# Optimization experiments

Hardware: AMD Instinct MI355X
Metric: run time of the kernel (lower is better)

## Reference

```python
import jax, jax.numpy as jnp
import numpy as np
from jax import lax

B, T, C = 4, 4096, 2048
H, Dh = 16, 128          # num_heads, head_dim
K = 4                    # depthwise conv kernel
LN_EPS = 1e-5
NORM_EPS = 1e-12         # F.normalize eps


def setup_inputs() -> dict:
    key = jax.random.key(0)
    ks = jax.random.split(key, 9)
    s = 0.02
    x = jax.random.normal(ks[0], (B, T, C), jnp.float32)
    Wq = jax.random.normal(ks[1], (C, C), jnp.float32) * s  # torch Linear weight [out,in]
    Wk = jax.random.normal(ks[2], (C, C), jnp.float32) * s
    Wv = jax.random.normal(ks[3], (C, C), jnp.float32) * s
    Wo = jax.random.normal(ks[4], (C, C), jnp.float32) * s
    conv_w = jax.random.normal(ks[5], (C, 1, K), jnp.float32) * 0.2  # depthwise [O, I/groups, K]
    conv_b = jax.random.normal(ks[6], (C,), jnp.float32) * s
    gate_w = jax.random.normal(ks[7], (C, C), jnp.float32) * s
    gate_b = jnp.zeros((C,), jnp.float32)                   # gate_bias_init = 0.0
    ln_w = jnp.ones((C,), jnp.float32)
    ln_b = jnp.zeros((C,), jnp.float32)
    g = jnp.linspace(0.9, 0.999, H, dtype=jnp.float32).at[0].set(1.0)
    gamma = g.reshape(1, 1, H, 1)                           # non-trainable buffer
    return {"x": x, "Wq": Wq, "Wk": Wk, "Wv": Wv, "Wo": Wo,
            "conv_w": conv_w, "conv_b": conv_b, "gate_w": gate_w, "gate_b": gate_b,
            "ln_w": ln_w, "ln_b": ln_b, "gamma": gamma}


def _l2norm(t):
    n = jnp.linalg.norm(t, axis=-1, keepdims=True)
    return t / jnp.maximum(n, NORM_EPS)


def reference(x, Wq, Wk, Wv, Wo, conv_w, conv_b, gate_w, gate_b, ln_w, ln_b, gamma):
    b, t, c = x.shape
    # causal depthwise conv (torch pads K-1 both sides then slices [:T] == left-pad K-1)
    xc = lax.conv_general_dilated(
        jnp.swapaxes(x, 1, 2), conv_w, window_strides=(1,), padding=[(K - 1, 0)],
        feature_group_count=c, dimension_numbers=("NCH", "OIH", "NCH"))
    x_conv = jax.nn.silu(jnp.swapaxes(xc + conv_b[None, :, None], 1, 2))  # [B,T,C]

    q = jnp.einsum("btc,dc->btd", x, Wq).reshape(b, t, H, Dh)
    k = jnp.einsum("btc,dc->btd", x, Wk).reshape(b, t, H, Dh)
    v = jnp.einsum("btc,dc->btd", x, Wv).reshape(b, t, H, Dh)
    gate = jax.nn.sigmoid(jnp.einsum("btc,dc->btd", x_conv, gate_w) + gate_b)
    gate = gate.reshape(b, t, H, Dh)

    q = _l2norm(q)
    k = _l2norm(k)

    # elementwise decayed scan: S_t = gamma * S_{t-1} + k_t * v_t ; mem_t = gate_t * S_t
    kv = jnp.swapaxes(k * v, 0, 1)          # [T,B,H,Dh]
    g = gamma.reshape(1, H, 1)

    def step(S, kv_t):
        S = g * S + kv_t
        return S, S

    _, S_seq = lax.scan(step, jnp.zeros((b, H, Dh), x.dtype), kv)
    mem = gate * jnp.swapaxes(S_seq, 0, 1)  # [B,T,H,Dh]

    out = (mem * q).reshape(b, t, c)
    y = jnp.einsum("btc,dc->btd", out, Wo)
    mu = jnp.mean(y, axis=-1, keepdims=True)
    var = jnp.mean(jnp.square(y - mu), axis=-1, keepdims=True)
    return (y - mu) * lax.rsqrt(var + LN_EPS) * ln_w + ln_b
```

## Files before the change

kernel.cpp:

```cpp
#include <hip/hip_runtime.h>
#include <cstdint>

#define Bb 4
#define Tt 4096
#define Cc 2048
#define Hh 16
#define Dh 128
#define BT (Bb * Tt)
#define NCHUNK 32
#define TCHUNK 128
#define NCHAN (Bb * Cc)
#define NQKV 6144

typedef __bf16 bf16x8 __attribute__((ext_vector_type(8)));
typedef float f32x4 __attribute__((ext_vector_type(4)));
typedef unsigned short u16x8 __attribute__((ext_vector_type(8)));

__device__ __forceinline__ float bf2f(unsigned short u) {
  return __uint_as_float(((unsigned)u) << 16);
}
__device__ __forceinline__ unsigned short f2bf(float f) {
  unsigned u = __float_as_uint(f);
  u = u + 0x7fffu + ((u >> 16) & 1u);
  return (unsigned short)(u >> 16);
}

__device__ __forceinline__ void async_copy16(void* lds, const void* gmem) {
  auto* lp = (__attribute__((address_space(3))) unsigned int*)(unsigned)(uintptr_t)(lds);
  auto* gp = (const __attribute__((address_space(1))) unsigned int*)(uintptr_t)(gmem);
  __builtin_amdgcn_global_load_lds(gp, lp, 16, 0, 0);
}

__global__ __launch_bounds__(256) void cvt5_kernel(const float* __restrict__ Wq,
                                                   const float* __restrict__ Wk,
                                                   const float* __restrict__ Wv,
                                                   const float* __restrict__ Wo,
                                                   const float* __restrict__ Wg,
                                                   unsigned short* __restrict__ dst) {
  size_t idx4 = ((size_t)blockIdx.x * 256 + threadIdx.x) * 4;
  int region = (int)(idx4 >> 22);
  size_t off = idx4 & ((1u << 22) - 1);
  const float* src;
  switch (region) {
    case 0: src = Wq; break;
    case 1: src = Wk; break;
    case 2: src = Wv; break;
    case 3: src = Wo; break;
    default: src = Wg; break;
  }
  float4 v = *(const float4*)(src + off);
  unsigned r0 = (unsigned)f2bf(v.x) | ((unsigned)f2bf(v.y) << 16);
  unsigned r1 = (unsigned)f2bf(v.z) | ((unsigned)f2bf(v.w) << 16);
  *(uint2*)(dst + idx4) = make_uint2(r0, r1);
}

__global__ __launch_bounds__(256) void conv_kernel(const float* __restrict__ x,
                                                   const float* __restrict__ cw,
                                                   const float* __restrict__ cb,
                                                   unsigned short* __restrict__ xb,
                                                   unsigned short* __restrict__ xcb) {
  int idx = blockIdx.x * 256 + threadIdx.x;
  int cg = idx & 511;
  int rg = idx >> 9;
  int c = cg * 4;
  size_t bt0 = (size_t)rg * 8;
  int t0 = (int)(bt0 & (Tt - 1));
  const float* xp = x + bt0 * Cc + c;

  float4 w4[4];
#pragma unroll
  for (int u = 0; u < 4; u++) w4[u] = *(const float4*)(cw + (size_t)(c + u) * 4);
  float4 bias = *(const float4*)(cb + c);
  const float* bs = (const float*)&bias;

  float xr[11][4];
  if (t0 != 0) {
#pragma unroll
    for (int j = 0; j < 3; j++) {
      float4 p = *(const float4*)(xp - (size_t)(3 - j) * Cc);
      xr[j][0] = p.x; xr[j][1] = p.y; xr[j][2] = p.z; xr[j][3] = p.w;
    }
  } else {
#pragma unroll
    for (int j = 0; j < 3; j++)
#pragma unroll
      for (int u = 0; u < 4; u++) xr[j][u] = 0.f;
  }
#pragma unroll
  for (int i = 0; i < 8; i++) {
    float4 p = *(const float4*)(xp + (size_t)i * Cc);
    xr[3 + i][0] = p.x; xr[3 + i][1] = p.y; xr[3 + i][2] = p.z; xr[3 + i][3] = p.w;
    unsigned a0 = (unsigned)f2bf(p.x) | ((unsigned)f2bf(p.y) << 16);
    unsigned a1 = (unsigned)f2bf(p.z) | ((unsigned)f2bf(p.w) << 16);
    *(uint2*)(xb + (bt0 + i) * Cc + c) = make_uint2(a0, a1);
  }
#pragma unroll
  for (int i = 0; i < 8; i++) {
    unsigned short o[4];
#pragma unroll
    for (int u = 0; u < 4; u++) {
      const float* wf = (const float*)&w4[u];
      float a = bs[u];
#pragma unroll
      for (int j = 0; j < 4; j++) a += wf[3 - j] * xr[3 + i - j][u];
      float sig = 1.f / (1.f + expf(-a));
      o[u] = f2bf(a * sig);
    }
    unsigned q0 = (unsigned)o[0] | ((unsigned)o[1] << 16);
    unsigned q1 = (unsigned)o[2] | ((unsigned)o[3] << 16);
    *(uint2*)(xcb + (bt0 + i) * Cc + c) = make_uint2(q0, q1);
  }
}

template <int EPI>
__global__ __launch_bounds__(512, 2) void gemm256(const unsigned short* __restrict__ A,
                                                  const unsigned short* __restrict__ B,
                                                  void* __restrict__ C,
                                                  const float* __restrict__ bias,
                                                  int M, int N, int K) {
  __shared__ unsigned short As[4][256 * 32];
  __shared__ unsigned short Bs[4][256 * 32];
  __shared__ float rowsq[256][4];

  const int tid = threadIdx.x;
  const int w = tid >> 6;
  const int lane = tid & 63;

  const int nwg = gridDim.x * gridDim.y;
  const int flat = blockIdx.y * gridDim.x + blockIdx.x;
  const int cpx = nwg >> 3;
  const int swz = (flat & 7) * cpx + (flat >> 3);
  const int bx = swz % gridDim.x;
  const int by = swz / gridDim.x;
  const int m0 = bx * 256;
  const int n0 = by * 256;

  const int wr = w >> 2;
  const int wc = w & 3;

  const int srow = lane >> 2;
  const int scol = (((lane & 3) ^ ((lane >> 3) & 3)) << 3);
  const int r16 = w * 2;
  const unsigned short* Ag0 = A + (size_t)(m0 + r16 * 16 + srow) * K + scol;
  const unsigned short* Ag1 = Ag0 + (size_t)16 * K;
  const unsigned short* Bg0 = B + (size_t)(n0 + r16 * 16 + srow) * K + scol;
  const unsigned short* Bg1 = Bg0 + (size_t)16 * K;

  const int frow = lane & 15;
  const int cbs = ((((lane >> 4) << 4) ^ (((frow >> 1) & 3) << 4)) >> 1);

  f32x4 acc[8][4] = {};
  const int NT = K >> 5;

  {
    unsigned short* dA0 = &As[0][r16 * 512];
    unsigned short* dB0 = &Bs[0][r16 * 512];
    async_copy16(dA0, Ag0); async_copy16(dA0 + 512, Ag1);
    async_copy16(dB0, Bg0); async_copy16(dB0 + 512, Bg1);
    unsigned short* dA1 = &As[1][r16 * 512];
    unsigned short* dB1 = &Bs[1][r16 * 512];
    async_copy16(dA1, Ag0 + 32); async_copy16(dA1 + 512, Ag1 + 32);
    async_copy16(dB1, Bg0 + 32); async_copy16(dB1 + 512, Bg1 + 32);
  }
  asm volatile("s_waitcnt vmcnt(4)" ::: "memory");
  __builtin_amdgcn_s_barrier();

  for (int t = 0; t < NT; ++t) {
    const int slot = t & 3;
    const unsigned short* as = &As[slot][0] + wr * 4096 + cbs;
    const unsigned short* bsb = &Bs[slot][0] + wc * 2048 + cbs;
    const bool pf = (t + 2 < NT);
    const int kpf = (t + 2) << 5;

    bf16x8 af[4], bf[4];
#pragma unroll
    for (int m = 0; m < 4; m++)
      af[m] = __builtin_bit_cast(bf16x8, *(const u16x8*)(as + (m * 16 + frow) * 32));
#pragma unroll
    for (int n = 0; n < 4; n++)
      bf[n] = __builtin_bit_cast(bf16x8, *(const u16x8*)(bsb + (n * 16 + frow) * 32));
    if (pf) {
      unsigned short* d = &As[(t + 2) & 3][r16 * 512];
      async_copy16(d, Ag0 + kpf);
      async_copy16(d + 512, Ag1 + kpf);
    }
    __builtin_amdgcn_s_barrier();
    asm volatile("s_waitcnt lgkmcnt(0)" ::: "memory");
    __builtin_amdgcn_sched_barrier(0);
    __builtin_amdgcn_s_setprio(1);
#pragma unroll
    for (int m = 0; m < 4; m++)
#pragma unroll
      for (int n = 0; n < 4; n++)
        acc[m][n] = __builtin_amdgcn_mfma_f32_16x16x32_bf16(af[m], bf[n], acc[m][n], 0, 0, 0);
    __builtin_amdgcn_s_setprio(0);
    __builtin_amdgcn_s_barrier();

#pragma unroll
    for (int m = 0; m < 4; m++)
      af[m] = __builtin_bit_cast(bf16x8, *(const u16x8*)(as + ((m + 4) * 16 + frow) * 32));
    if (pf) {
      unsigned short* d = &Bs[(t + 2) & 3][r16 * 512];
      async_copy16(d, Bg0 + kpf);
      async_copy16(d + 512, Bg1 + kpf);
    }
    __builtin_amdgcn_s_barrier();
    asm volatile("s_waitcnt lgkmcnt(0)" ::: "memory");
    __builtin_amdgcn_sched_barrier(0);
    __builtin_amdgcn_s_setprio(1);
#pragma unroll
    for (int m = 0; m < 4; m++)
#pragma unroll
      for (int n = 0; n < 4; n++)
        acc[m + 4][n] = __builtin_amdgcn_mfma_f32_16x16x32_bf16(af[m], bf[n], acc[m + 4][n], 0, 0, 0);
    __builtin_amdgcn_s_setprio(0);
    if (pf) asm volatile("s_waitcnt vmcnt(4)" ::: "memory");
    else    asm volatile("s_waitcnt vmcnt(0)" ::: "memory");
    __builtin_amdgcn_s_barrier();
  }

  const int crow0 = (lane >> 4) * 4;
  const int ccol = lane & 15;

  float inv[8][4];
  const bool donorm = (EPI == 3) && (n0 < 2 * Cc);
  if (donorm) {
#pragma unroll
    for (int m = 0; m < 8; m++) {
#pragma unroll
      for (int r = 0; r < 4; r++) {
        float sq = 0.f;
#pragma unroll
        for (int n = 0; n < 4; n++) { float v = acc[m][n][r]; sq += v * v; }
        sq += __shfl_xor(sq, 1);
        sq += __shfl_xor(sq, 2);
        sq += __shfl_xor(sq, 4);
        sq += __shfl_xor(sq, 8);
        if (ccol == 0) rowsq[wr * 128 + m * 16 + crow0 + r][wc] = sq;
      }
    }
    __syncthreads();
#pragma unroll
    for (int m = 0; m < 8; m++)
#pragma unroll
      for (int r = 0; r < 4; r++) {
        int rloc = wr * 128 + m * 16 + crow0 + r;
        int g2 = (wc >> 1) * 2;
        float s = rowsq[rloc][g2] + rowsq[rloc][g2 + 1];
        inv[m][r] = 1.f / fmaxf(sqrtf(s), 1e-12f);
      }
  }

#pragma unroll
  for (int m = 0; m < 8; m++) {
#pragma unroll
    for (int n = 0; n < 4; n++) {
      int col = n0 + wc * 64 + n * 16 + ccol;
      float bv = (EPI == 1) ? bias[col] : 0.f;
#pragma unroll
      for (int r = 0; r < 4; r++) {
        int row = m0 + wr * 128 + m * 16 + crow0 + r;
        float v = acc[m][n][r];
        if (EPI == 1) v = 1.f / (1.f + expf(-(v + bv)));
        if (donorm) v *= inv[m][r];
        if (EPI == 2)
          ((float*)C)[(size_t)row * N + col] = v;
        else
          ((unsigned short*)C)[(size_t)row * N + col] = f2bf(v);
      }
    }
  }
}

__global__ __launch_bounds__(256) void scan_p1(const unsigned short* __restrict__ qkv,
                                               const float* __restrict__ gamma,
                                               float* __restrict__ carry) {
  int idx = blockIdx.x * 256 + threadIdx.x;
  int ch4 = idx & 2047;
  int chunk = idx >> 11;
  int b = ch4 >> 9;
  int c = (ch4 & 511) * 4;
  float g = gamma[c >> 7];
  const unsigned short* kb = qkv + ((size_t)(b * Tt + chunk * TCHUNK)) * NQKV + Cc + c;
  float L[4] = {0.f, 0.f, 0.f, 0.f};
#pragma unroll 4
  for (int t = 0; t < TCHUNK; t++) {
    const unsigned short* p = kb + (size_t)t * NQKV;
    uint2 kk = *(const uint2*)(p);
    uint2 vv = *(const uint2*)(p + Cc);
    L[0] = g * L[0] + bf2f((unsigned short)(kk.x & 0xffff)) * bf2f((unsigned short)(vv.x & 0xffff));
    L[1] = g * L[1] + bf2f((unsigned short)(kk.x >> 16))    * bf2f((unsigned short)(vv.x >> 16));
    L[2] = g * L[2] + bf2f((unsigned short)(kk.y & 0xffff)) * bf2f((unsigned short)(vv.y & 0xffff));
    L[3] = g * L[3] + bf2f((unsigned short)(kk.y >> 16))    * bf2f((unsigned short)(vv.y >> 16));
  }
  *(float4*)(carry + (size_t)chunk * NCHAN + b * Cc + c) = make_float4(L[0], L[1], L[2], L[3]);
}

__global__ __launch_bounds__(256) void scan_p2(float* __restrict__ carry,
                                               const float* __restrict__ gamma) {
  int ch = blockIdx.x * 256 + threadIdx.x;
  int h = (ch & (Cc - 1)) >> 7;
  float g = gamma[h];
  float gTc = g;
#pragma unroll
  for (int i = 0; i < 7; i++) gTc *= gTc;
  float E = 0.f;
  for (int cidx = 0; cidx < NCHUNK; cidx++) {
    float L = carry[(size_t)cidx * NCHAN + ch];
    carry[(size_t)cidx * NCHAN + ch] = E;
    E = gTc * E + L;
  }
}

__global__ __launch_bounds__(256) void scan_p3(const unsigned short* __restrict__ qkv,
                                               unsigned short* __restrict__ gb,
                                               const float* __restrict__ gamma,
                                               const float* __restrict__ carry) {
  int idx = blockIdx.x * 256 + threadIdx.x;
  int ch4 = idx & 2047;
  int chunk = idx >> 11;
  int b = ch4 >> 9;
  int c = (ch4 & 511) * 4;
  float g = gamma[c >> 7];
  float4 Sv = *(const float4*)(carry + (size_t)chunk * NCHAN + b * Cc + c);
  float S[4] = {Sv.x, Sv.y, Sv.z, Sv.w};
  const unsigned short* qb = qkv + ((size_t)(b * Tt + chunk * TCHUNK)) * NQKV + c;
  unsigned short* gp = gb + ((size_t)(b * Tt + chunk * TCHUNK)) * Cc + c;
#pragma unroll 4
  for (int t = 0; t < TCHUNK; t++) {
    const unsigned short* p = qb + (size_t)t * NQKV;
    uint2 qq = *(const uint2*)(p);
    uint2 kk = *(const uint2*)(p + Cc);
    uint2 vv = *(const uint2*)(p + 2 * Cc);
    uint2 gg = *(const uint2*)(gp + (size_t)t * Cc);
    float q0 = bf2f((unsigned short)(qq.x & 0xffff)), q1 = bf2f((unsigned short)(qq.x >> 16));
    float q2 = bf2f((unsigned short)(qq.y & 0xffff)), q3 = bf2f((unsigned short)(qq.y >> 16));
    float k0 = bf2f((unsigned short)(kk.x & 0xffff)), k1 = bf2f((unsigned short)(kk.x >> 16));
    float k2 = bf2f((unsigned short)(kk.y & 0xffff)), k3 = bf2f((unsigned short)(kk.y >> 16));
    float v0 = bf2f((unsigned short)(vv.x & 0xffff)), v1 = bf2f((unsigned short)(vv.x >> 16));
    float v2 = bf2f((unsigned short)(vv.y & 0xffff)), v3 = bf2f((unsigned short)(vv.y >> 16));
    float g0 = bf2f((unsigned short)(gg.x & 0xffff)), g1 = bf2f((unsigned short)(gg.x >> 16));
    float g2 = bf2f((unsigned short)(gg.y & 0xffff)), g3 = bf2f((unsigned short)(gg.y >> 16));
    S[0] = g * S[0] + k0 * v0;
    S[1] = g * S[1] + k1 * v1;
    S[2] = g * S[2] + k2 * v2;
    S[3] = g * S[3] + k3 * v3;
    unsigned short o0 = f2bf(g0 * S[0] * q0);
    unsigned short o1 = f2bf(g1 * S[1] * q1);
    unsigned short o2 = f2bf(g2 * S[2] * q2);
    unsigned short o3 = f2bf(g3 * S[3] * q3);
    *(uint2*)(gp + (size_t)t * Cc) =
        make_uint2((unsigned)o0 | ((unsigned)o1 << 16), (unsigned)o2 | ((unsigned)o3 << 16));
  }
}

__global__ __launch_bounds__(256) void ln_kernel(float* __restrict__ y,
                                                 const float* __restrict__ w,
                                                 const float* __restrict__ b) {
  float* p = y + (size_t)blockIdx.x * Cc;
  int tid = threadIdx.x;
  float v[8];
  float s = 0.f, sq = 0.f;
#pragma unroll
  for (int i = 0; i < 8; i++) {
    v[i] = p[tid + i * 256];
    s += v[i];
    sq += v[i] * v[i];
  }
#pragma unroll
  for (int o = 32; o > 0; o >>= 1) { s += __shfl_down(s, o); sq += __shfl_down(sq, o); }
  __shared__ float ss[4], ssq[4];
  int wave = tid >> 6, lane = tid & 63;
  if (lane == 0) { ss[wave] = s; ssq[wave] = sq; }
  __syncthreads();
  s = ss[0] + ss[1] + ss[2] + ss[3];
  sq = ssq[0] + ssq[1] + ssq[2] + ssq[3];
  float mu = s * (1.f / (float)Cc);
  float var = fmaxf(sq * (1.f / (float)Cc) - mu * mu, 0.f);
  float rs = rsqrtf(var + 1e-5f);
#pragma unroll
  for (int i = 0; i < 8; i++) {
    int c = tid + i * 256;
    p[c] = (v[i] - mu) * rs * w[c] + b[c];
  }
}

extern "C" void kernel_launch(void* const* d_in, const int* in_sizes, int n_in,
                              void* d_out, int out_size, void* d_ws, size_t ws_size,
                              hipStream_t stream) {
  const float* x      = (const float*)d_in[0];
  const float* Wq     = (const float*)d_in[1];
  const float* Wk     = (const float*)d_in[2];
  const float* Wv     = (const float*)d_in[3];
  const float* Wo     = (const float*)d_in[4];
  const float* conv_w = (const float*)d_in[5];
  const float* conv_b = (const float*)d_in[6];
  const float* gate_w = (const float*)d_in[7];
  const float* gate_b = (const float*)d_in[8];
  const float* ln_w   = (const float*)d_in[9];
  const float* ln_b   = (const float*)d_in[10];
  const float* gamma  = (const float*)d_in[11];

  char* ws = (char*)d_ws;
  const size_t SZ_BTC = (size_t)BT * Cc * 2;
  const size_t SZ_W   = (size_t)Cc * Cc * 2;
  unsigned short* xb   = (unsigned short*)(ws);
  unsigned short* xcb  = (unsigned short*)(ws + SZ_BTC);
  unsigned short* wb   = (unsigned short*)(ws + 2 * SZ_BTC);
  unsigned short* qkvb = (unsigned short*)(ws + 2 * SZ_BTC + 5 * SZ_W);
  unsigned short* gb   = (unsigned short*)(ws + 2 * SZ_BTC + 5 * SZ_W + 3 * SZ_BTC);
  float* carry         = (float*)(ws + 2 * SZ_BTC + 5 * SZ_W + 4 * SZ_BTC);

  unsigned short* wob = wb + 3 * (size_t)Cc * Cc;
  unsigned short* wgb = wb + 4 * (size_t)Cc * Cc;

  const int nW = Cc * Cc;
  cvt5_kernel<<<5 * nW / 1024, 256, 0, stream>>>(Wq, Wk, Wv, Wo, gate_w, wb);
  conv_kernel<<<(BT / 8) * (Cc / 4) / 256, 256, 0, stream>>>(x, conv_w, conv_b, xb, xcb);

  dim3 gqkv(BT / 256, NQKV / 256);
  gemm256<3><<<gqkv, 512, 0, stream>>>(xb, wb, qkvb, nullptr, BT, NQKV, Cc);

  dim3 ggrid(BT / 256, Cc / 256);
  gemm256<1><<<ggrid, 512, 0, stream>>>(xcb, wgb, gb, gate_b, BT, Cc, Cc);

  scan_p1<<<(NCHUNK * NCHAN / 4) / 256, 256, 0, stream>>>(qkvb, gamma, carry);
  scan_p2<<<NCHAN / 256, 256, 0, stream>>>(carry, gamma);
  scan_p3<<<(NCHUNK * NCHAN / 4) / 256, 256, 0, stream>>>(qkvb, gb, gamma, carry);

  gemm256<2><<<ggrid, 512, 0, stream>>>(gb, wob, d_out, nullptr, BT, Cc, Cc);
  ln_kernel<<<BT, 256, 0, stream>>>((float*)d_out, ln_w, ln_b);
}
```

Measured before the change: 1.194 ms.

## Software-pipeline LDS fragment loads across k-tiles with double-buffered B registers

Restructures the GEMM main loop so the A and B fragments for the next k-tile are read from LDS while the second half of the current tile's MFMAs is still in flight. B fragments are held in two register sets that alternate across a 2x-unrolled loop. All four global-to-LDS async copies for tile t+2 are issued together at the start of each step. The intent is to hide LDS read latency behind MFMA work, at the cost of extra VGPRs and partial lgkmcnt waits that must stay correct. The unrolled-by-two loop assumes NT is even.

```diff
diff --git a/kernel.cpp b/kernel.cpp
--- a/kernel.cpp
+++ b/kernel.cpp
@@ -165,59 +165,79 @@
   asm volatile("s_waitcnt vmcnt(4)" ::: "memory");
   __builtin_amdgcn_s_barrier();
 
-  for (int t = 0; t < NT; ++t) {
-    const int slot = t & 3;
-    const unsigned short* as = &As[slot][0] + wr * 4096 + cbs;
-    const unsigned short* bsb = &Bs[slot][0] + wc * 2048 + cbs;
-    const bool pf = (t + 2 < NT);
-    const int kpf = (t + 2) << 5;
-
-    bf16x8 af[4], bf[4];
+  bf16x8 afA[4], afB[4], bfq0[4], bfq1[4];
+  {
+    const unsigned short* as0 = &As[0][0] + wr * 4096 + cbs;
+    const unsigned short* bs0 = &Bs[0][0] + wc * 2048 + cbs;
 #pragma unroll
     for (int m = 0; m < 4; m++)
-      af[m] = __builtin_bit_cast(bf16x8, *(const u16x8*)(as + (m * 16 + frow) * 32));
+      afA[m] = __builtin_bit_cast(bf16x8, *(const u16x8*)(as0 + (m * 16 + frow) * 32));
 #pragma unroll
     for (int n = 0; n < 4; n++)
-      bf[n] = __builtin_bit_cast(bf16x8, *(const u16x8*)(bsb + (n * 16 + frow) * 32));
-    if (pf) {
-      unsigned short* d = &As[(t + 2) & 3][r16 * 512];
-      async_copy16(d, Ag0 + kpf);
-      async_copy16(d + 512, Ag1 + kpf);
-    }
-    __builtin_amdgcn_s_barrier();
-    asm volatile("s_waitcnt lgkmcnt(0)" ::: "memory");
-    __builtin_amdgcn_sched_barrier(0);
-    __builtin_amdgcn_s_setprio(1);
-#pragma unroll
-    for (int m = 0; m < 4; m++)
-#pragma unroll
-      for (int n = 0; n < 4; n++)
-        acc[m][n] = __builtin_amdgcn_mfma_f32_16x16x32_bf16(af[m], bf[n], acc[m][n], 0, 0, 0);
-    __builtin_amdgcn_s_setprio(0);
-    __builtin_amdgcn_s_barrier();
-
-#pragma unroll
-    for (int m = 0; m < 4; m++)
-      af[m] = __builtin_bit_cast(bf16x8, *(const u16x8*)(as + ((m + 4) * 16 + frow) * 32));
-    if (pf) {
-      unsigned short* d = &Bs[(t + 2) & 3][r16 * 512];
-      async_copy16(d, Bg0 + kpf);
-      async_copy16(d + 512, Bg1 + kpf);
-    }
-    __builtin_amdgcn_s_barrier();
-    asm volatile("s_waitcnt lgkmcnt(0)" ::: "memory");
-    __builtin_amdgcn_sched_barrier(0);
-    __builtin_amdgcn_s_setprio(1);
-#pragma unroll
-    for (int m = 0; m < 4; m++)
-#pragma unroll
-      for (int n = 0; n < 4; n++)
-        acc[m + 4][n] = __builtin_amdgcn_mfma_f32_16x16x32_bf16(af[m], bf[n], acc[m + 4][n], 0, 0, 0);
-    __builtin_amdgcn_s_setprio(0);
-    if (pf) asm volatile("s_waitcnt vmcnt(4)" ::: "memory");
-    else    asm volatile("s_waitcnt vmcnt(0)" ::: "memory");
-    __builtin_amdgcn_s_barrier();
-  }
+      bfq0[n] = __builtin_bit_cast(bf16x8, *(const u16x8*)(bs0 + (n * 16 + frow) * 32));
+  }
+
+#define TILE_STEP(T, BFCUR, BFNXT)                                                         \
+  do {                                                                                     \
+    const int slot_ = (T) & 3;                                                             \
+    const unsigned short* asw_ = &As[slot_][0] + wr * 4096 + cbs;                          \
+    const bool pf_ = (T) + 2 < NT;                                                         \
+    const bool rd_ = (T) + 1 < NT;                                                         \
+                                                                    \
+    if (pf_) {                                                                             \
+      const int kpf_ = ((T) + 2) << 5;                                                     \
+      unsigned short* dA_ = &As[((T) + 2) & 3][r16 * 512];                                 \
+      unsigned short* dB_ = &Bs[((T) + 2) & 3][r16 * 512];                                 \
+      async_copy16(dA_, Ag0 + kpf_); async_copy16(dA_ + 512, Ag1 + kpf_);                  \
+      async_copy16(dB_, Bg0 + kpf_); async_copy16(dB_ + 512, Bg1 + kpf_);                  \
+    }                                                                                      \
+    _Pragma("unroll")                                                                      \
+    for (int m = 0; m < 4; m++)                                                            \
+      afB[m] = __builtin_bit_cast(bf16x8, *(const u16x8*)(asw_ + ((m + 4) * 16 + frow) * 32)); \
+    __builtin_amdgcn_s_barrier();                                                          \
+    asm volatile("s_waitcnt lgkmcnt(4)" ::: "memory");                                     \
+    __builtin_amdgcn_sched_barrier(0);                                                     \
+    __builtin_amdgcn_s_setprio(1);                                                         \
+    _Pragma("unroll")                                                                      \
+    for (int m = 0; m < 4; m++)                                                            \
+      _Pragma("unroll")                                                                    \
+      for (int n = 0; n < 4; n++)                                                          \
+        acc[m][n] = __builtin_amdgcn_mfma_f32_16x16x32_bf16(afA[m], BFCUR[n], acc[m][n], 0, 0, 0); \
+    __builtin_amdgcn_s_setprio(0);                                                         \
+    if (pf_) asm volatile("s_waitcnt vmcnt(4)" ::: "memory");                              \
+    else     asm volatile("s_waitcnt vmcnt(0)" ::: "memory");                              \
+    __builtin_amdgcn_s_barrier();                                                          \
+                                                                    \
+    if (rd_) {                                                                             \
+      const int slot1_ = ((T) + 1) & 3;                                                    \
+      const unsigned short* asn_ = &As[slot1_][0] + wr * 4096 + cbs;                       \
+      const unsigned short* bsn_ = &Bs[slot1_][0] + wc * 2048 + cbs;                       \
+      _Pragma("unroll")                                                                    \
+      for (int m = 0; m < 4; m++)                                                          \
+        afA[m] = __builtin_bit_cast(bf16x8, *(const u16x8*)(asn_ + (m * 16 + frow) * 32)); \
+      _Pragma("unroll")                                                                    \
+      for (int n = 0; n < 4; n++)                                                          \
+        BFNXT[n] = __builtin_bit_cast(bf16x8, *(const u16x8*)(bsn_ + (n * 16 + frow) * 32)); \
+    }                                                                                      \
+    __builtin_amdgcn_s_barrier();                                                          \
+    if (rd_) asm volatile("s_waitcnt lgkmcnt(8)" ::: "memory");                            \
+    else     asm volatile("s_waitcnt lgkmcnt(0)" ::: "memory");                            \
+    __builtin_amdgcn_sched_barrier(0);                                                     \
+    __builtin_amdgcn_s_setprio(1);                                                         \
+    _Pragma("unroll")                                                                      \
+    for (int m = 0; m < 4; m++)                                                            \
+      _Pragma("unroll")                                                                    \
+      for (int n = 0; n < 4; n++)                                                          \
+        acc[m + 4][n] = __builtin_amdgcn_mfma_f32_16x16x32_bf16(afB[m], BFCUR[n], acc[m + 4][n], 0, 0, 0); \
+    __builtin_amdgcn_s_setprio(0);                                                         \
+    __builtin_amdgcn_s_barrier();                                                          \
+  } while (0)
+
+  for (int tt = 0; tt < NT; tt += 2) {
+    TILE_STEP(tt, bfq0, bfq1);
+    TILE_STEP(tt + 1, bfq1, bfq0);
+  }
+#undef TILE_STEP
 
   const int crow0 = (lane >> 4) * 4;
   const int ccol = lane & 15;
```

Result: slower. 1.220 ms (+2.2%).
